# Performance work log

Hardware: AMD Instinct MI355X
Metric: run time of the kernel (lower is better)

The kernel has to match this reference:

```python
import jax, jax.numpy as jnp
import numpy as np

IN_FEATURES = 1024
OUT_FEATURES = 128


def setup_inputs() -> dict:
    key = jax.random.key(0)
    k1, k2, k3, k4, k5 = jax.random.split(key, 5)
    B, T, E, D = 4, 4096, IN_FEATURES, OUT_FEATURES
    s_in = 1.0 / np.sqrt(E)
    s_d = 1.0 / np.sqrt(D)
    return {
        "x": jax.random.normal(k1, (B, T, E), dtype=jnp.float32),
        "Wk": jax.random.uniform(k2, (E, D), jnp.float32, -s_in, s_in),
        "Wq": jax.random.uniform(k3, (E, D), jnp.float32, -s_in, s_in),
        "Wv": jax.random.uniform(k4, (E, D), jnp.float32, -s_in, s_in),
        "Wp": jax.random.uniform(k5, (D, D), jnp.float32, -s_d, s_d),
    }


def reference(x, Wk, Wq, Wv, Wp):
    # x: [B, T, E]; projections stored as [in, out] (torch Linear transposed)
    B, T, E = x.shape
    D = Wk.shape[1]
    k = x @ Wk  # [B, T, D]
    q = x @ Wq
    v = x @ Wv
    scale = 1.0 / jnp.sqrt(jnp.asarray(D, x.dtype))
    attn = jnp.einsum("btd,bsd->bts", q, k) * scale  # [B, T, T]
    causal = jnp.tril(jnp.ones((T, T), dtype=bool))
    attn = jnp.where(causal, attn, -jnp.inf)
    attn = jax.nn.softmax(attn, axis=-1)
    out = jnp.einsum("bts,bsd->btd", attn, v)  # [B, T, D]
    return out @ Wp  # dropout p=0.0 -> identity
```

## Files before the change

### kernel.cpp

```cpp
#include <hip/hip_runtime.h>

#define E_DIM 1024
#define D_DIM 128
#define T_DIM 4096

typedef unsigned short u16;
typedef u16 u16x8 __attribute__((ext_vector_type(8)));
typedef u16 u16x4 __attribute__((ext_vector_type(4)));
typedef __bf16 bf16x8 __attribute__((ext_vector_type(8)));
typedef float f32x4 __attribute__((ext_vector_type(4)));

__device__ __forceinline__ u16 cvt_bf16(float f) {
    unsigned u = __float_as_uint(f);
    u += 0x7FFF + ((u >> 16) & 1);
    return (u16)(u >> 16);
}

__device__ __forceinline__ float bf2f(u16 v) {
    return __uint_as_float(((unsigned)v) << 16);
}

__device__ __forceinline__ f32x4 mfma16(u16x8 a, u16x8 b, f32x4 c) {
    return __builtin_amdgcn_mfma_f32_16x16x32_bf16(
        __builtin_bit_cast(bf16x8, a), __builtin_bit_cast(bf16x8, b), c, 0, 0, 0);
}

__device__ __forceinline__ void gld_lds16(const void* g, void* l) {
    __builtin_amdgcn_global_load_lds(
        (const __attribute__((address_space(1))) unsigned int*)g,
        (__attribute__((address_space(3))) unsigned int*)l, 16, 0, 0);
}

__global__ void prep_kernel(const float* __restrict__ Wk, const float* __restrict__ Wq,
                            const float* __restrict__ Wv, const float* __restrict__ Wp,
                            u16* __restrict__ Wqt, u16* __restrict__ Wkt,
                            u16* __restrict__ Wvt, u16* __restrict__ Wpt) {
    int tid = blockIdx.x * 256 + threadIdx.x;
    const int WT = 128 * 1024;
    if (tid < 3 * WT) {
        int w = tid / WT;
        int r = tid - w * WT;
        int n = r >> 10, k = r & 1023;
        const float* W = (w == 0) ? Wq : (w == 1) ? Wk : Wv;
        u16* Wt = (w == 0) ? Wqt : (w == 1) ? Wkt : Wvt;
        Wt[r] = cvt_bf16(W[k * 128 + n]);
    } else {
        int r = tid - 3 * WT;
        if (r < 128 * 128) {
            int n = r >> 7, k = r & 127;
            Wpt[r] = cvt_bf16(Wp[k * 128 + n]);
        }
    }
}

__global__ __launch_bounds__(512) void qkv_kernel(
        const float* __restrict__ x,
        const u16* __restrict__ Wqt, const u16* __restrict__ Wkt, const u16* __restrict__ Wvt,
        u16* __restrict__ qb, u16* __restrict__ kb, u16* __restrict__ vT) {
    __shared__ __align__(16) char smem[73728];

    const int t = threadIdx.x;
    const int w = t >> 6;
    const int lane = t & 63;
    const int lr = lane & 15;
    const int lg = lane >> 4;
    const int m4 = w & 3;
    const int n2 = w >> 2;
    const int r0 = blockIdx.x * 64;

    #define STAGE_W(K0, BUF) do {                                                 \
        char* wB_ = smem + (BUF) * 24576;                                         \
        _Pragma("unroll")                                                         \
        for (int c2 = 0; c2 < 3; ++c2) {                                          \
            const int rl_ = c2 * 128 + (t >> 2);                                  \
            const u16* W_ = (rl_ < 128) ? Wqt : (rl_ < 256) ? Wkt : Wvt;          \
            const int s_ = ((t & 3) - (rl_ >> 1)) & 3;                            \
            gld_lds16(W_ + (size_t)(rl_ & 127) * E_DIM + (K0) + 8 * s_,           \
                      wB_ + c2 * 8192 + t * 16);                                  \
        }                                                                         \
    } while (0)

    const float* xp = x + (size_t)(r0 + 16 * m4 + lr) * E_DIM + lg * 8;

    float4 x0[2], x1[2], x2[2];
    #define XLOAD(arr, K0) do {                                                   \
        arr[0] = *(const float4*)(xp + (K0));                                     \
        arr[1] = *(const float4*)(xp + (K0) + 4);                                 \
    } while (0)

    #define CVT_AV(av, arr) do {                                                  \
        av[0] = cvt_bf16(arr[0].x); av[1] = cvt_bf16(arr[0].y);                   \
        av[2] = cvt_bf16(arr[0].z); av[3] = cvt_bf16(arr[0].w);                   \
        av[4] = cvt_bf16(arr[1].x); av[5] = cvt_bf16(arr[1].y);                   \
        av[6] = cvt_bf16(arr[1].z); av[7] = cvt_bf16(arr[1].w);                   \
    } while (0)

    f32x4 acc[12];
    #pragma unroll
    for (int j = 0; j < 12; ++j) acc[j] = f32x4{0.f, 0.f, 0.f, 0.f};

    #define ITER(KK, BUF, SBUF, XC, XN) do {                                      \
        const int kk_ = (KK);                                                     \
        u16x8 av_;                                                                \
        CVT_AV(av_, XC);                                                          \
        __builtin_amdgcn_sched_barrier(0);                                        \
        if (kk_ < 30) {                                                           \
            STAGE_W(kk_ * 32 + 64, SBUF);                                         \
            __builtin_amdgcn_sched_barrier(0);                                    \
            XLOAD(XN, kk_ * 32 + 64);                                             \
        }                                                                         \
        __builtin_amdgcn_sched_barrier(0);                                        \
        {                                                                         \
            char* wB = smem + (BUF) * 24576;                                      \
            __builtin_amdgcn_s_setprio(1);                                        \
            _Pragma("unroll")                                                     \
            for (int nt = 0; nt < 12; ++nt) {                                     \
                const int ln = n2 * 192 + nt * 16 + lr;                           \
                u16x8 bv = *(u16x8*)(wB + ln * 64 + (((lg + (ln >> 1)) & 3) << 4)); \
                acc[nt] = mfma16(av_, bv, acc[nt]);                               \
            }                                                                     \
            __builtin_amdgcn_s_setprio(0);                                        \
        }                                                                         \
        if (kk_ < 30) asm volatile("s_waitcnt vmcnt(5)" ::: "memory");            \
        else          asm volatile("s_waitcnt vmcnt(0)" ::: "memory");            \
        __builtin_amdgcn_s_barrier();                                             \
    } while (0)

    STAGE_W(0, 0);
    XLOAD(x0, 0);
    STAGE_W(32, 1);
    XLOAD(x1, 32);
    asm volatile("s_waitcnt vmcnt(5)" ::: "memory");
    __builtin_amdgcn_s_barrier();

    for (int kk = 0; kk < 30; kk += 3) {
        ITER(kk,     0, 2, x0, x2);
        ITER(kk + 1, 1, 0, x1, x0);
        ITER(kk + 2, 2, 1, x2, x1);
    }
    ITER(30, 0, 2, x0, x2);
    ITER(31, 1, 0, x1, x0);
    #undef STAGE_W
    #undef XLOAD
    #undef CVT_AV
    #undef ITER

    const float qscale = 0.12752048520120164f;
    const int bb = r0 >> 12;
    const int row0 = r0 + 16 * m4 + 4 * lg;
    const int tt0 = row0 & 4095;
    #pragma unroll
    for (int nt = 0; nt < 12; ++nt) {
        const int col_g = n2 * 192 + nt * 16 + lr;
        const int j = col_g >> 7;
        const int colw = col_g & 127;
        if (j < 2) {
            u16* outb = (j == 0) ? qb : kb;
            const float sc = (j == 0) ? qscale : 1.0f;
            #pragma unroll
            for (int reg = 0; reg < 4; ++reg)
                outb[(size_t)(row0 + reg) * D_DIM + colw] = cvt_bf16(acc[nt][reg] * sc);
        } else {
            u16x4 pv;
            #pragma unroll
            for (int reg = 0; reg < 4; ++reg) pv[reg] = cvt_bf16(acc[nt][reg]);
            *(u16x4*)&vT[((size_t)(bb * 128 + colw)) * T_DIM + tt0] = pv;
        }
    }
}

__global__ __launch_bounds__(512) void attn_kernel(
        const u16* __restrict__ qb, const u16* __restrict__ kb, const u16* __restrict__ vT,
        u16* __restrict__ Opart, float* __restrict__ ml, int SPLIT) {
    const int g = blockIdx.x;
    const int b = blockIdx.y;
    int i, c;
    if (SPLIT) {
        int k = 0;
        while (2 * (k + 1) * (k + 2) <= g) ++k;
        const int off = g - 2 * k * (k + 1);
        const int iband = off / (k + 1);
        c = off - iband * (k + 1);
        i = 4 * k + iband;
    } else { i = g; c = 0; }

    const int q0 = i * 128;
    const int kv_beg = c * 512;
    const int kv_end = SPLIT ? min(q0 + 128, kv_beg + 512) : (q0 + 128);
    const int slot = b * gridDim.x + g;

    __shared__ __align__(16) char smem[81920];

    const int t = threadIdx.x;
    const int w = t >> 6;
    const int lane = t & 63;
    const int lr = lane & 15;
    const int lg = lane >> 4;
    const size_t base = (size_t)b * T_DIM * D_DIM;

    u16x8 qf[4];
    {
        const u16* qp = qb + base + (size_t)(q0 + 16 * w + lr) * D_DIM + lg * 8;
        #pragma unroll
        for (int dk = 0; dk < 4; ++dk) qf[dk] = *(const u16x8*)(qp + dk * 32);
    }

    const char* kpb = (const char*)(kb + base);
    const char* vpb = (const char*)(vT + (size_t)b * D_DIM * T_DIM);
    const int key = (lr & 7) << 4;

    #define STAGE(S0, BUF) do {                                                   \
        char* kB_ = smem + (BUF) * 16384;                                         \
        char* vB_ = smem + 32768 + (BUF) * 16384;                                 \
        const int wbase_ = (t >> 6) * 1024;                                       \
        _Pragma("unroll")                                                         \
        for (int c2 = 0; c2 < 2; ++c2) {                                          \
            const int krow_ = c2 * 32 + (t >> 4);                                 \
            gld_lds16(kpb + (size_t)((S0) + krow_) * 256 +                        \
                      (((t & 15) * 16) ^ ((krow_ & 7) * 16)),                     \
                      kB_ + c2 * 8192 + wbase_);                                  \
            const int vrow_ = c2 * 64 + (t >> 3);                                 \
            gld_lds16(vpb + (size_t)vrow_ * (T_DIM * 2) + (size_t)(S0) * 2 +      \
                      (((t & 7) * 16) ^ ((vrow_ & 7) * 16)),                      \
                      vB_ + c2 * 8192 + wbase_);                                  \
        }                                                                         \
    } while (0)

    f32x4 oacc[8];
    #pragma unroll
    for (int nn = 0; nn < 8; ++nn) oacc[nn] = f32x4{0.f, 0.f, 0.f, 0.f};
    float m_run = -1e30f, l_run = 0.f;
    const int qrow = q0 + 16 * w + lr;
    const int qmax = q0 + 16 * w + 15;

    STAGE(kv_beg, 0);
    asm volatile("s_waitcnt vmcnt(0)" ::: "memory");
    __syncthreads();

    int buf = 0;
    for (int s0 = kv_beg; s0 < kv_end; s0 += 64) {
        if (s0 + 64 < kv_end) STAGE(s0 + 64, buf ^ 1);

        if (s0 <= qmax) {
            char* kB  = smem + buf * 16384;
            char* vB  = smem + 32768 + buf * 16384;
            char* psB = smem + 65536 + w * 2048;

            f32x4 sacc[4];
            #pragma unroll
            for (int nn = 0; nn < 4; ++nn) sacc[nn] = f32x4{0.f, 0.f, 0.f, 0.f};
            __builtin_amdgcn_s_setprio(1);
            #pragma unroll
            for (int dk = 0; dk < 4; ++dk) {
                #pragma unroll
                for (int nt = 0; nt < 4; ++nt) {
                    u16x8 kfr = *(u16x8*)(kB + (nt * 16 + lr) * 256 + ((dk * 64 + lg * 16) ^ key));
                    sacc[nt] = mfma16(kfr, qf[dk], sacc[nt]);
                }
            }
            __builtin_amdgcn_s_setprio(0);

            float sv[4][4];
            const bool need_mask = (s0 + 63 > q0 + 16 * w);
            #pragma unroll
            for (int nt = 0; nt < 4; ++nt) {
                #pragma unroll
                for (int r = 0; r < 4; ++r) {
                    float v = sacc[nt][r];
                    if (need_mask && (s0 + nt * 16 + 4 * lg + r) > qrow) v = -1e30f;
                    sv[nt][r] = v;
                }
            }

            float tmax = sv[0][0];
            #pragma unroll
            for (int nt = 0; nt < 4; ++nt)
                #pragma unroll
                for (int r = 0; r < 4; ++r) tmax = fmaxf(tmax, sv[nt][r]);
            tmax = fmaxf(tmax, __shfl_xor(tmax, 16));
            tmax = fmaxf(tmax, __shfl_xor(tmax, 32));

            if (!__all(tmax <= m_run + 8.0f)) {
                float m_new = fmaxf(m_run, tmax);
                float rsc = __builtin_amdgcn_exp2f(m_run - m_new);
                m_run = m_new;
                l_run *= rsc;
                #pragma unroll
                for (int nt = 0; nt < 8; ++nt)
                    #pragma unroll
                    for (int r = 0; r < 4; ++r) oacc[nt][r] *= rsc;
            }

            float tsum = 0.f;
            #pragma unroll
            for (int nt = 0; nt < 4; ++nt)
                #pragma unroll
                for (int r = 0; r < 4; ++r) {
                    sv[nt][r] = __builtin_amdgcn_exp2f(sv[nt][r] - m_run);
                    tsum += sv[nt][r];
                }
            tsum += __shfl_xor(tsum, 16);
            tsum += __shfl_xor(tsum, 32);
            l_run += tsum;

            #pragma unroll
            for (int nt = 0; nt < 4; ++nt) {
                u16x4 pv4;
                #pragma unroll
                for (int r = 0; r < 4; ++r) pv4[r] = cvt_bf16(sv[nt][r]);
                *(u16x4*)(psB + lr * 128 + ((nt * 32 + lg * 8) ^ key)) = pv4;
            }

            u16x8 pA0 = *(u16x8*)(psB + lr * 128 + ((lg * 16) ^ key));
            u16x8 pA1 = *(u16x8*)(psB + lr * 128 + ((64 + lg * 16) ^ key));

            __builtin_amdgcn_s_setprio(1);
            #pragma unroll
            for (int nt = 0; nt < 8; ++nt) {
                u16x8 bv0 = *(u16x8*)(vB + (nt * 16 + lr) * 128 + ((lg * 16) ^ key));
                oacc[nt] = mfma16(bv0, pA0, oacc[nt]);
                u16x8 bv1 = *(u16x8*)(vB + (nt * 16 + lr) * 128 + ((64 + lg * 16) ^ key));
                oacc[nt] = mfma16(bv1, pA1, oacc[nt]);
            }
            __builtin_amdgcn_s_setprio(0);
        }

        asm volatile("s_waitcnt vmcnt(0)" ::: "memory");
        __syncthreads();
        buf ^= 1;
    }
    #undef STAGE

    if (lg == 0) {
        int row = 16 * w + lr;
        ml[(size_t)(slot * 128 + row) * 2]     = m_run;
        ml[(size_t)(slot * 128 + row) * 2 + 1] = l_run;
    }

    const float invl = 1.f / l_run;
    const int orw = 16 * w + lr;
    #pragma unroll
    for (int nt = 0; nt < 8; ++nt) {
        u16x4 ov;
        #pragma unroll
        for (int r = 0; r < 4; ++r) ov[r] = cvt_bf16(oacc[nt][r] * invl);
        *(u16x4*)(smem + orw * 256 + ((32 * nt + 8 * lg) ^ ((orw & 7) << 4))) = ov;
    }
    __syncthreads();
    u16* op = Opart + (size_t)slot * 16384;
    const int orow = t >> 2;
    const int oseg = t & 3;
    #pragma unroll
    for (int j = 0; j < 4; ++j) {
        u16x8 vv = *(u16x8*)(smem + orow * 256 + ((oseg * 64 + j * 16) ^ ((orow & 7) << 4)));
        *(u16x8*)(op + orow * 128 + oseg * 32 + j * 8) = vv;
    }
}

__global__ __launch_bounds__(256) void combine_kernel(
        const u16* __restrict__ Opart, const float* __restrict__ ml,
        const u16* __restrict__ Wpt, float* __restrict__ out,
        int SPLIT, int NSLOT) {
    const int io = blockIdx.x;
    const int b = blockIdx.y;
    const int i = io >> 1;
    const int half = io & 1;
    int NC, g0;
    if (SPLIT) {
        int k = i >> 2;
        NC = k + 1;
        g0 = 2 * k * (k + 1) + (i & 3) * (k + 1);
    } else { NC = 1; g0 = i; }
    const int slot0 = b * NSLOT + g0;

    __shared__ u16 Os[64][136];
    const int t = threadIdx.x;
    const int row = t >> 2, seg = (t & 3) * 32;
    const int row_in = half * 64 + row;

    float m_fin = -1e30f;
    for (int c = 0; c < NC; ++c)
        m_fin = fmaxf(m_fin, ml[(size_t)((slot0 + c) * 128 + row_in) * 2]);

    float acc[32];
    #pragma unroll
    for (int j = 0; j < 32; ++j) acc[j] = 0.f;
    float l_fin = 0.f;
    for (int c = 0; c < NC; ++c) {
        float mcv = ml[(size_t)((slot0 + c) * 128 + row_in) * 2];
        float lcv = ml[(size_t)((slot0 + c) * 128 + row_in) * 2 + 1];
        float wgt = __builtin_amdgcn_exp2f(mcv - m_fin) * lcv;
        l_fin += wgt;
        const u16* opc = Opart + (size_t)(slot0 + c) * 16384 + row_in * 128 + seg;
        #pragma unroll
        for (int j = 0; j < 4; ++j) {
            u16x8 v = *(const u16x8*)(opc + j * 8);
            #pragma unroll
            for (int e = 0; e < 8; ++e)
                acc[j * 8 + e] += bf2f(v[e]) * wgt;
        }
    }
    const float inv = 1.f / l_fin;

    #pragma unroll
    for (int j = 0; j < 4; ++j) {
        u16x8 ov;
        #pragma unroll
        for (int e = 0; e < 8; ++e) ov[e] = cvt_bf16(acc[j * 8 + e] * inv);
        *(u16x8*)&Os[row][seg + j * 8] = ov;
    }
    __syncthreads();

    const int w = t >> 6;
    const int lane = t & 63;
    const int lr = lane & 15;
    const int lg = lane >> 4;
    u16x8 af[4];
    #pragma unroll
    for (int dk = 0; dk < 4; ++dk)
        af[dk] = *(u16x8*)&Os[16 * w + lr][dk * 32 + lg * 8];
    float* op = out + ((size_t)b * T_DIM + io * 64) * D_DIM;
    #pragma unroll
    for (int nt = 0; nt < 8; ++nt) {
        f32x4 y = f32x4{0.f, 0.f, 0.f, 0.f};
        #pragma unroll
        for (int dk = 0; dk < 4; ++dk) {
            u16x8 bv = *(const u16x8*)&Wpt[(size_t)(nt * 16 + lr) * D_DIM + dk * 32 + lg * 8];
            y = mfma16(af[dk], bv, y);
        }
        #pragma unroll
        for (int r = 0; r < 4; ++r)
            op[(size_t)(16 * w + 4 * lg + r) * D_DIM + nt * 16 + lr] = y[r];
    }
}

extern "C" void kernel_launch(void* const* d_in, const int* in_sizes, int n_in,
                              void* d_out, int out_size, void* d_ws, size_t ws_size,
                              hipStream_t stream) {
    const float* x  = (const float*)d_in[0];
    const float* Wk = (const float*)d_in[1];
    const float* Wq = (const float*)d_in[2];
    const float* Wv = (const float*)d_in[3];
    const float* Wp = (const float*)d_in[4];
    float* out = (float*)d_out;

    char* ws = (char*)d_ws;
    u16* qb  = (u16*)(ws);
    u16* kb  = (u16*)(ws + 4194304);
    u16* vT  = (u16*)(ws + 8388608);
    u16* Wqt = (u16*)(ws + 12582912);
    u16* Wkt = (u16*)(ws + 12582912 + 262144);
    u16* Wvt = (u16*)(ws + 12582912 + 524288);
    u16* Wpt = (u16*)(ws + 12582912 + 786432);
    float* ml   = (float*)(ws + 13631488);
    u16* Opart  = (u16*)(ws + 14680064);

    const bool big = ws_size >= (size_t)36 * 1024 * 1024;
    const int SPLIT = big ? 1 : 0;
    const int GX = big ? 144 : 32;

    prep_kernel<<<1600, 256, 0, stream>>>(Wk, Wq, Wv, Wp, Wqt, Wkt, Wvt, Wpt);
    qkv_kernel<<<256, 512, 0, stream>>>(x, Wqt, Wkt, Wvt, qb, kb, vT);
    attn_kernel<<<dim3(GX, 4), 512, 0, stream>>>(qb, kb, vT, Opart, ml, SPLIT);
    combine_kernel<<<dim3(64, 4), 256, 0, stream>>>(Opart, ml, Wpt, out, SPLIT, GX);
}
```

Before: 98.35 us.

## Give each attention wave two 16-row query tiles with 256-thread blocks

The attention kernel now runs with 4 waves of 256 threads instead of 8 waves, and each wave handles 32 query rows as two 16-row halves. Each K and V fragment read from LDS is reused for two MFMAs, which halves LDS fragment traffic per unit of compute, and the staging loop is reorganised so fewer threads cover the same tiles. The cost is roughly doubled accumulator and register pressure per wave and fewer waves per block to hide latency. The coarser causal-skip granularity can also waste some work on diagonal tiles.

```diff
diff --git a/kernel.cpp b/kernel.cpp
--- a/kernel.cpp
+++ b/kernel.cpp
@@ -169,7 +169,7 @@
     }
 }
 
-__global__ __launch_bounds__(512) void attn_kernel(
+__global__ __launch_bounds__(256) void attn_kernel(
         const u16* __restrict__ qb, const u16* __restrict__ kb, const u16* __restrict__ vT,
         u16* __restrict__ Opart, float* __restrict__ ml, int SPLIT) {
     const int g = blockIdx.x;
@@ -198,11 +198,12 @@
     const int lg = lane >> 4;
     const size_t base = (size_t)b * T_DIM * D_DIM;
 
-    u16x8 qf[4];
-    {
-        const u16* qp = qb + base + (size_t)(q0 + 16 * w + lr) * D_DIM + lg * 8;
-        #pragma unroll
-        for (int dk = 0; dk < 4; ++dk) qf[dk] = *(const u16x8*)(qp + dk * 32);
+    u16x8 qf[2][4];
+    #pragma unroll
+    for (int h = 0; h < 2; ++h) {
+        const u16* qp = qb + base + (size_t)(q0 + 32 * w + 16 * h + lr) * D_DIM + lg * 8;
+        #pragma unroll
+        for (int dk = 0; dk < 4; ++dk) qf[h][dk] = *(const u16x8*)(qp + dk * 32);
     }
 
     const char* kpb = (const char*)(kb + base);
@@ -212,26 +213,26 @@
     #define STAGE(S0, BUF) do {                                                   \
         char* kB_ = smem + (BUF) * 16384;                                         \
         char* vB_ = smem + 32768 + (BUF) * 16384;                                 \
-        const int wbase_ = (t >> 6) * 1024;                                       \
         _Pragma("unroll")                                                         \
-        for (int c2 = 0; c2 < 2; ++c2) {                                          \
-            const int krow_ = c2 * 32 + (t >> 4);                                 \
+        for (int c2 = 0; c2 < 4; ++c2) {                                          \
+            const int krow_ = c2 * 16 + (t >> 4);                                 \
             gld_lds16(kpb + (size_t)((S0) + krow_) * 256 +                        \
                       (((t & 15) * 16) ^ ((krow_ & 7) * 16)),                     \
-                      kB_ + c2 * 8192 + wbase_);                                  \
-            const int vrow_ = c2 * 64 + (t >> 3);                                 \
+                      kB_ + c2 * 4096 + t * 16);                                  \
+            const int vrow_ = c2 * 32 + (t >> 3);                                 \
             gld_lds16(vpb + (size_t)vrow_ * (T_DIM * 2) + (size_t)(S0) * 2 +      \
                       (((t & 7) * 16) ^ ((vrow_ & 7) * 16)),                      \
-                      vB_ + c2 * 8192 + wbase_);                                  \
+                      vB_ + c2 * 4096 + t * 16);                                  \
         }                                                                         \
     } while (0)
 
-    f32x4 oacc[8];
-    #pragma unroll
-    for (int nn = 0; nn < 8; ++nn) oacc[nn] = f32x4{0.f, 0.f, 0.f, 0.f};
-    float m_run = -1e30f, l_run = 0.f;
-    const int qrow = q0 + 16 * w + lr;
-    const int qmax = q0 + 16 * w + 15;
+    f32x4 oacc[2][8];
+    #pragma unroll
+    for (int h = 0; h < 2; ++h)
+        #pragma unroll
+        for (int nn = 0; nn < 8; ++nn) oacc[h][nn] = f32x4{0.f, 0.f, 0.f, 0.f};
+    float m_run[2] = {-1e30f, -1e30f}, l_run[2] = {0.f, 0.f};
+    const int qmax = q0 + 32 * w + 31;
 
     STAGE(kv_beg, 0);
     asm volatile("s_waitcnt vmcnt(0)" ::: "memory");
@@ -244,83 +245,93 @@
         if (s0 <= qmax) {
             char* kB  = smem + buf * 16384;
             char* vB  = smem + 32768 + buf * 16384;
-            char* psB = smem + 65536 + w * 2048;
-
-            f32x4 sacc[4];
-            #pragma unroll
-            for (int nn = 0; nn < 4; ++nn) sacc[nn] = f32x4{0.f, 0.f, 0.f, 0.f};
+            char* psB = smem + 65536 + w * 4096;
+
+            f32x4 sacc[2][4];
+            #pragma unroll
+            for (int h = 0; h < 2; ++h)
+                #pragma unroll
+                for (int nn = 0; nn < 4; ++nn) sacc[h][nn] = f32x4{0.f, 0.f, 0.f, 0.f};
             __builtin_amdgcn_s_setprio(1);
             #pragma unroll
             for (int dk = 0; dk < 4; ++dk) {
                 #pragma unroll
                 for (int nt = 0; nt < 4; ++nt) {
                     u16x8 kfr = *(u16x8*)(kB + (nt * 16 + lr) * 256 + ((dk * 64 + lg * 16) ^ key));
-                    sacc[nt] = mfma16(kfr, qf[dk], sacc[nt]);
+                    sacc[0][nt] = mfma16(kfr, qf[0][dk], sacc[0][nt]);
+                    sacc[1][nt] = mfma16(kfr, qf[1][dk], sacc[1][nt]);
                 }
             }
             __builtin_amdgcn_s_setprio(0);
 
-            float sv[4][4];
-            const bool need_mask = (s0 + 63 > q0 + 16 * w);
-            #pragma unroll
-            for (int nt = 0; nt < 4; ++nt) {
-                #pragma unroll
-                for (int r = 0; r < 4; ++r) {
-                    float v = sacc[nt][r];
-                    if (need_mask && (s0 + nt * 16 + 4 * lg + r) > qrow) v = -1e30f;
-                    sv[nt][r] = v;
+            #pragma unroll
+            for (int h = 0; h < 2; ++h) {
+                const int qrow = q0 + 32 * w + 16 * h + lr;
+                const bool need_mask = (s0 + 63 > q0 + 32 * w + 16 * h);
+                float sv[4][4];
+                #pragma unroll
+                for (int nt = 0; nt < 4; ++nt)
+                    #pragma unroll
+                    for (int r = 0; r < 4; ++r) {
+                        float v = sacc[h][nt][r];
+                        if (need_mask && (s0 + nt * 16 + 4 * lg + r) > qrow) v = -1e30f;
+                        sv[nt][r] = v;
+                    }
+
+                float tmax = sv[0][0];
+                #pragma unroll
+                for (int nt = 0; nt < 4; ++nt)
+                    #pragma unroll
+                    for (int r = 0; r < 4; ++r) tmax = fmaxf(tmax, sv[nt][r]);
+                tmax = fmaxf(tmax, __shfl_xor(tmax, 16));
+                tmax = fmaxf(tmax, __shfl_xor(tmax, 32));
+
+                if (!__all(tmax <= m_run[h] + 8.0f)) {
+                    float m_new = fmaxf(m_run[h], tmax);
+                    float rsc = __builtin_amdgcn_exp2f(m_run[h] - m_new);
+                    m_run[h] = m_new;
+                    l_run[h] *= rsc;
+                    #pragma unroll
+                    for (int nt = 0; nt < 8; ++nt)
+                        #pragma unroll
+                        for (int r = 0; r < 4; ++r) oacc[h][nt][r] *= rsc;
+                }
+
+                float tsum = 0.f;
+                #pragma unroll
+                for (int nt = 0; nt < 4; ++nt)
+                    #pragma unroll
+                    for (int r = 0; r < 4; ++r) {
+                        sv[nt][r] = __builtin_amdgcn_exp2f(sv[nt][r] - m_run[h]);
+                        tsum += sv[nt][r];
+                    }
+                tsum += __shfl_xor(tsum, 16);
+                tsum += __shfl_xor(tsum, 32);
+                l_run[h] += tsum;
+
+                #pragma unroll
+                for (int nt = 0; nt < 4; ++nt) {
+                    u16x4 pv4;
+                    #pragma unroll
+                    for (int r = 0; r < 4; ++r) pv4[r] = cvt_bf16(sv[nt][r]);
+                    *(u16x4*)(psB + (16 * h + lr) * 128 + ((nt * 32 + lg * 8) ^ key)) = pv4;
                 }
             }
 
-            float tmax = sv[0][0];
-            #pragma unroll
-            for (int nt = 0; nt < 4; ++nt)
-                #pragma unroll
-                for (int r = 0; r < 4; ++r) tmax = fmaxf(tmax, sv[nt][r]);
-            tmax = fmaxf(tmax, __shfl_xor(tmax, 16));
-            tmax = fmaxf(tmax, __shfl_xor(tmax, 32));
-
-            if (!__all(tmax <= m_run + 8.0f)) {
-                float m_new = fmaxf(m_run, tmax);
-                float rsc = __builtin_amdgcn_exp2f(m_run - m_new);
-                m_run = m_new;
-                l_run *= rsc;
-                #pragma unroll
-                for (int nt = 0; nt < 8; ++nt)
-                    #pragma unroll
-                    for (int r = 0; r < 4; ++r) oacc[nt][r] *= rsc;
-            }
-
-            float tsum = 0.f;
-            #pragma unroll
-            for (int nt = 0; nt < 4; ++nt)
-                #pragma unroll
-                for (int r = 0; r < 4; ++r) {
-                    sv[nt][r] = __builtin_amdgcn_exp2f(sv[nt][r] - m_run);
-                    tsum += sv[nt][r];
-                }
-            tsum += __shfl_xor(tsum, 16);
-            tsum += __shfl_xor(tsum, 32);
-            l_run += tsum;
-
-            #pragma unroll
-            for (int nt = 0; nt < 4; ++nt) {
-                u16x4 pv4;
-                #pragma unroll
-                for (int r = 0; r < 4; ++r) pv4[r] = cvt_bf16(sv[nt][r]);
-                *(u16x4*)(psB + lr * 128 + ((nt * 32 + lg * 8) ^ key)) = pv4;
-            }
-
-            u16x8 pA0 = *(u16x8*)(psB + lr * 128 + ((lg * 16) ^ key));
-            u16x8 pA1 = *(u16x8*)(psB + lr * 128 + ((64 + lg * 16) ^ key));
+            u16x8 pA0h0 = *(u16x8*)(psB + lr * 128 + ((lg * 16) ^ key));
+            u16x8 pA1h0 = *(u16x8*)(psB + lr * 128 + ((64 + lg * 16) ^ key));
+            u16x8 pA0h1 = *(u16x8*)(psB + (16 + lr) * 128 + ((lg * 16) ^ key));
+            u16x8 pA1h1 = *(u16x8*)(psB + (16 + lr) * 128 + ((64 + lg * 16) ^ key));
 
             __builtin_amdgcn_s_setprio(1);
             #pragma unroll
             for (int nt = 0; nt < 8; ++nt) {
                 u16x8 bv0 = *(u16x8*)(vB + (nt * 16 + lr) * 128 + ((lg * 16) ^ key));
-                oacc[nt] = mfma16(bv0, pA0, oacc[nt]);
+                oacc[0][nt] = mfma16(bv0, pA0h0, oacc[0][nt]);
+                oacc[1][nt] = mfma16(bv0, pA0h1, oacc[1][nt]);
                 u16x8 bv1 = *(u16x8*)(vB + (nt * 16 + lr) * 128 + ((64 + lg * 16) ^ key));
-                oacc[nt] = mfma16(bv1, pA1, oacc[nt]);
+                oacc[0][nt] = mfma16(bv1, pA1h0, oacc[0][nt]);
+                oacc[1][nt] = mfma16(bv1, pA1h1, oacc[1][nt]);
             }
             __builtin_amdgcn_s_setprio(0);
         }
@@ -332,28 +343,34 @@
     #undef STAGE
 
     if (lg == 0) {
-        int row = 16 * w + lr;
-        ml[(size_t)(slot * 128 + row) * 2]     = m_run;
-        ml[(size_t)(slot * 128 + row) * 2 + 1] = l_run;
-    }
-
-    const float invl = 1.f / l_run;
-    const int orw = 16 * w + lr;
-    #pragma unroll
-    for (int nt = 0; nt < 8; ++nt) {
-        u16x4 ov;
-        #pragma unroll
-        for (int r = 0; r < 4; ++r) ov[r] = cvt_bf16(oacc[nt][r] * invl);
-        *(u16x4*)(smem + orw * 256 + ((32 * nt + 8 * lg) ^ ((orw & 7) << 4))) = ov;
+        #pragma unroll
+        for (int h = 0; h < 2; ++h) {
+            int row = 32 * w + 16 * h + lr;
+            ml[(size_t)(slot * 128 + row) * 2]     = m_run[h];
+            ml[(size_t)(slot * 128 + row) * 2 + 1] = l_run[h];
+        }
+    }
+
+    #pragma unroll
+    for (int h = 0; h < 2; ++h) {
+        const float invl = 1.f / l_run[h];
+        const int orw = 32 * w + 16 * h + lr;
+        #pragma unroll
+        for (int nt = 0; nt < 8; ++nt) {
+            u16x4 ov;
+            #pragma unroll
+            for (int r = 0; r < 4; ++r) ov[r] = cvt_bf16(oacc[h][nt][r] * invl);
+            *(u16x4*)(smem + orw * 256 + ((32 * nt + 8 * lg) ^ ((orw & 7) << 4))) = ov;
+        }
     }
     __syncthreads();
     u16* op = Opart + (size_t)slot * 16384;
-    const int orow = t >> 2;
-    const int oseg = t & 3;
-    #pragma unroll
-    for (int j = 0; j < 4; ++j) {
-        u16x8 vv = *(u16x8*)(smem + orow * 256 + ((oseg * 64 + j * 16) ^ ((orow & 7) << 4)));
-        *(u16x8*)(op + orow * 128 + oseg * 32 + j * 8) = vv;
+    const int orow = t >> 1;
+    const int ohb = (t & 1) * 128;
+    #pragma unroll
+    for (int j = 0; j < 8; ++j) {
+        u16x8 vv = *(u16x8*)(smem + orow * 256 + ((ohb + j * 16) ^ ((orow & 7) << 4)));
+        *(u16x8*)(op + orow * 128 + (t & 1) * 64 + j * 8) = vv;
     }
 }
 
@@ -461,6 +478,6 @@
 
     prep_kernel<<<1600, 256, 0, stream>>>(Wk, Wq, Wv, Wp, Wqt, Wkt, Wvt, Wpt);
     qkv_kernel<<<256, 512, 0, stream>>>(x, Wqt, Wkt, Wvt, qb, kb, vT);
-    attn_kernel<<<dim3(GX, 4), 512, 0, stream>>>(qb, kb, vT, Opart, ml, SPLIT);
+    attn_kernel<<<dim3(GX, 4), 256, 0, stream>>>(qb, kb, vT, Opart, ml, SPLIT);
     combine_kernel<<<dim3(64, 4), 256, 0, stream>>>(Opart, ml, Wpt, out, SPLIT, GX);
 }
```

New measurement: 122.7 us. 1.25x slower.
